# Kernel optimization log

Measured on AMD Instinct MI355X. Metric: run time of the kernel, lower is better.

Reference implementation:

```python
import jax, jax.numpy as jnp
import numpy as np
from jax import lax

K = 16
SIGMA2 = 1.0  # sigma=1.0 squared
EPS = 1e-06


def setup_inputs() -> dict:
    key = jax.random.key(0)
    xyz = jax.random.normal(key, (4, 3, 4096), dtype=jnp.float32)
    return {"xyz": xyz}


def reference(xyz):
    # xyz: (B, 3, N)
    B, _, N = xyz.shape
    pts = jnp.transpose(xyz, (0, 2, 1))  # (B, N, 3)

    sq = jnp.sum(pts * pts, axis=-1)  # (B, N)
    d2 = sq[:, :, None] + sq[:, None, :] - 2.0 * jnp.einsum("bnd,bmd->bnm", pts, pts)

    # k nearest neighbors (smallest distance, includes self like torch knn on same set)
    _, idx = lax.top_k(-d2, K)  # idx: (B, N, K)

    # gather neighbor coordinates and recompute exact squared distance (faithful to source)
    neighbors = jax.vmap(lambda p, i: p[i])(pts, idx)  # (B, N, K, 3)
    diff = pts[:, :, None, :] - neighbors
    dist2 = jnp.sum(diff * diff, axis=-1)  # (B, N, K)
    weights = jnp.exp(-dist2 / (2.0 * SIGMA2))

    # scatter k-sparse weights into dense adjacency (topk indices per row are unique)
    bb = jnp.arange(B)[:, None, None]
    ii = jnp.arange(N)[None, :, None]
    A = jnp.zeros((B, N, N), dtype=xyz.dtype).at[bb, ii, idx].set(weights)
    A = 0.5 * (A + jnp.swapaxes(A, 1, 2))

    # symmetric normalized Laplacian L = I - D^{-1/2} A D^{-1/2} (diag scaling via broadcast)
    D = jnp.clip(jnp.sum(A, axis=-1), EPS, None)
    d_is = D ** -0.5  # (B, N)
    L = jnp.eye(N, dtype=xyz.dtype)[None] - d_is[:, :, None] * A * d_is[:, None, :]
    return L
```

## Files before the change

kernel.cpp:

```cpp
#include <hip/hip_runtime.h>
#include <math.h>

#pragma clang fp contract(off)

#define NPTS 4096
#define KNN  16
#define RPBK 16
#define KT   1024
#define CAP  128

__device__ __forceinline__ unsigned okey(float f) {
    f = f + 0.0f;
    unsigned u = __float_as_uint(f);
    return u ^ (((unsigned)((int)u >> 31)) | 0x80000000u);
}

__device__ __forceinline__ unsigned wmin32(unsigned v) {
    for (int o = 32; o > 0; o >>= 1) { unsigned w = __shfl_xor(v, o); v = w < v ? w : v; }
    return v;
}
__device__ __forceinline__ unsigned long long wmin64(unsigned long long v) {
    for (int o = 32; o > 0; o >>= 1) { unsigned long long w = __shfl_xor(v, o); v = w < v ? w : v; }
    return v;
}

__global__ void zero_kernel(float* __restrict__ p, int n) {
    int i = blockIdx.x * blockDim.x + threadIdx.x;
    if (i < n) p[i] = 0.0f;
}

__global__ __launch_bounds__(KT, 8) void knn_kernel(const float* __restrict__ xyz,
                                                    float* __restrict__ Dsum,
                                                    int* __restrict__ idx_out,
                                                    float* __restrict__ w_out) {
    __shared__ float4 spts[NPTS];
    __shared__ int    lists[RPBK][CAP];

    const int t    = threadIdx.x;
    const int lane = t & 63;
    const int wv   = t >> 6;
    const int rowg = blockIdx.x * RPBK + wv;
    const int b    = rowg >> 12;
    const float* X = xyz + (size_t)b * 3 * NPTS;

    for (int i = t; i < NPTS; i += KT) {
        float x = X[i], y = X[NPTS + i], z = X[2 * NPTS + i];
        spts[i] = make_float4(x, y, z, (x * x + y * y) + z * z);
    }
    __syncthreads();

    const float4 P = spts[rowg & (NPTS - 1)];

    unsigned best1 = 0xFFFFFFFFu;
    for (int i = 0; i < NPTS / 64; ++i) {
        float4 Q  = spts[i * 64 + lane];
        float dot = (P.x * Q.x + P.y * Q.y) + P.z * Q.z;
        float d2  = (P.w + Q.w) - 2.0f * dot;
        unsigned k = okey(d2);
        best1 = k < best1 ? k : best1;
    }
    unsigned cur = best1, T = 0;
    for (int r = 0; r < KNN; ++r) {
        unsigned mn = wmin32(cur);
        T = mn;
        if (cur == mn) cur = 0xFFFFFFFFu;
    }

    int cnt = 0;
    for (int i = 0; i < NPTS / 64; ++i) {
        int m = i * 64 + lane;
        float4 Q  = spts[m];
        float dot = (P.x * Q.x + P.y * Q.y) + P.z * Q.z;
        float d2  = (P.w + Q.w) - 2.0f * dot;
        bool pass = okey(d2) <= T;
        unsigned long long bal = __ballot(pass);
        if (pass) {
            int pos = cnt + __popcll(bal & ((1ull << lane) - 1ull));
            if (pos < CAP) lists[wv][pos] = m;
        }
        cnt += (int)__popcll(bal);
    }

    unsigned long long sel = ~0ull;
    if (cnt <= CAP) {
        unsigned long long e0 = ~0ull, e1 = ~0ull;
        if (lane < cnt) {
            int m = lists[wv][lane]; float4 Q = spts[m];
            float dot = (P.x * Q.x + P.y * Q.y) + P.z * Q.z;
            float d2  = (P.w + Q.w) - 2.0f * dot;
            e0 = ((unsigned long long)okey(d2) << 32) | (unsigned)m;
        }
        if (lane + 64 < cnt) {
            int m = lists[wv][lane + 64]; float4 Q = spts[m];
            float dot = (P.x * Q.x + P.y * Q.y) + P.z * Q.z;
            float d2  = (P.w + Q.w) - 2.0f * dot;
            e1 = ((unsigned long long)okey(d2) << 32) | (unsigned)m;
        }
        unsigned long long c = e0 < e1 ? e0 : e1;
        for (int r = 0; r < KNN; ++r) {
            unsigned long long mn = wmin64(c);
            if (c == mn) {
                if (e0 == mn) e0 = ~0ull; else e1 = ~0ull;
                c = e0 < e1 ? e0 : e1;
            }
            if (lane == r) sel = mn;
        }
    } else {
        unsigned long long last = 0;
        for (int r = 0; r < KNN; ++r) {
            unsigned long long bestp = ~0ull;
            for (int i = 0; i < NPTS / 64; ++i) {
                int m = i * 64 + lane;
                float4 Q  = spts[m];
                float dot = (P.x * Q.x + P.y * Q.y) + P.z * Q.z;
                float d2  = (P.w + Q.w) - 2.0f * dot;
                unsigned long long key = ((unsigned long long)okey(d2) << 32) | (unsigned)m;
                if (key > last && key < bestp) bestp = key;
            }
            unsigned long long mn = wmin64(bestp);
            if (lane == r) sel = mn;
            last = mn;
        }
    }

    float wgt = 0.0f;
    if (lane < KNN) {
        int j = (int)(unsigned)(sel & 0xFFFFFFFFull);
        float4 Q = spts[j];
        float dx = P.x - Q.x, dy = P.y - Q.y, dz = P.z - Q.z;
        float dist2 = (dx * dx + dy * dy) + dz * dz;
        wgt = expf(-(dist2 * 0.5f));
        size_t base = (size_t)rowg * KNN + lane;
        idx_out[base] = j;
        w_out[base]   = wgt;
        atomicAdd(&Dsum[(b << 12) + j], 0.5f * wgt);
    }
    float rs = wgt;
    for (int o = 32; o > 0; o >>= 1) rs += __shfl_xor(rs, o);
    if (lane == 0) atomicAdd(&Dsum[rowg], 0.5f * rs);
}

__global__ void dis_kernel(const float* __restrict__ Dsum, float* __restrict__ dis, int n) {
    int i = blockIdx.x * blockDim.x + threadIdx.x;
    if (i < n) dis[i] = 1.0f / sqrtf(fmaxf(Dsum[i], 1e-6f));
}

__global__ __launch_bounds__(256) void fill_kernel(float4* __restrict__ L4, size_t T4) {
    size_t g4     = (size_t)blockIdx.x * blockDim.x + threadIdx.x;
    size_t stride = (size_t)gridDim.x * blockDim.x;
    for (; g4 < T4; g4 += stride) {
        size_t g = g4 << 2;
        int o    = (int)(g & (size_t)(NPTS * (size_t)NPTS - 1));
        int row  = o >> 12;
        int col0 = o & (NPTS - 1);
        float4 v;
        v.x = (row == col0    ) ? 1.0f : 0.0f;
        v.y = (row == col0 + 1) ? 1.0f : 0.0f;
        v.z = (row == col0 + 2) ? 1.0f : 0.0f;
        v.w = (row == col0 + 3) ? 1.0f : 0.0f;
        L4[g4] = v;
    }
}

__global__ __launch_bounds__(256) void scatter_kernel(const int* __restrict__ idxb,
                                                      const float* __restrict__ wb,
                                                      const float* __restrict__ dis,
                                                      float* __restrict__ L) {
    int g   = blockIdx.x * 256 + threadIdx.x;
    int row = g >> 4;
    int b   = row >> 12;
    int n   = row & (NPTS - 1);
    int j   = idxb[g];
    float v = -0.5f * wb[g] * dis[row] * dis[(b << 12) + j];
    float* Lb = L + (size_t)b * NPTS * NPTS;
    atomicAdd(Lb + (size_t)n * NPTS + j, v);
    atomicAdd(Lb + (size_t)j * NPTS + n, v);
}

extern "C" void kernel_launch(void* const* d_in, const int* in_sizes, int n_in,
                              void* d_out, int out_size, void* d_ws, size_t ws_size,
                              hipStream_t stream) {
    const float* xyz = (const float*)d_in[0];
    const int B  = in_sizes[0] / (3 * NPTS);
    const int BN = B * NPTS;

    float* Dsum = (float*)d_ws;
    float* dis  = Dsum + BN;
    int*   idxb = (int*)(dis + BN);
    float* wb   = (float*)(idxb + (size_t)BN * KNN);
    float* L    = (float*)d_out;

    zero_kernel<<<BN / 256, 256, 0, stream>>>(Dsum, BN);
    knn_kernel<<<BN / RPBK, KT, 0, stream>>>(xyz, Dsum, idxb, wb);
    dis_kernel<<<BN / 256, 256, 0, stream>>>(Dsum, dis, BN);
    size_t T4 = (size_t)B * NPTS * NPTS / 4;
    fill_kernel<<<8192, 256, 0, stream>>>((float4*)d_out, T4);
    scatter_kernel<<<(BN * KNN) / 256, 256, 0, stream>>>(idxb, wb, dis, L);
}
```

Baseline: 369.6 us.

## Process two rows per wave in kNN and fuse zero/dis kernels into neighbors

Each wave in the kNN kernel now handles two query rows, sharing each shared-memory point load across both distance computations in the threshold and filter passes. Blocks shrink to 8 waves. The Dsum zeroing moves into the fill kernel and the inverse-sqrt degree computation moves into the scatter kernel, removing two small launches. The risks are more register pressure per thread and a hardcoded zeroing size that assumes the batch fits in 4096 float4s.

```diff
diff --git a/kernel.cpp b/kernel.cpp
--- a/kernel.cpp
+++ b/kernel.cpp
@@ -5,8 +5,10 @@
 
 #define NPTS 4096
 #define KNN  16
-#define RPBK 16
-#define KT   1024
+#define RPW  2
+#define KWAVES 8
+#define KT   (KWAVES * 64)
+#define RPBK (KWAVES * RPW)
 #define CAP  128
 
 __device__ __forceinline__ unsigned okey(float f) {
@@ -24,130 +26,12 @@
     return v;
 }
 
-__global__ void zero_kernel(float* __restrict__ p, int n) {
-    int i = blockIdx.x * blockDim.x + threadIdx.x;
-    if (i < n) p[i] = 0.0f;
-}
-
-__global__ __launch_bounds__(KT, 8) void knn_kernel(const float* __restrict__ xyz,
-                                                    float* __restrict__ Dsum,
-                                                    int* __restrict__ idx_out,
-                                                    float* __restrict__ w_out) {
-    __shared__ float4 spts[NPTS];
-    __shared__ int    lists[RPBK][CAP];
-
-    const int t    = threadIdx.x;
-    const int lane = t & 63;
-    const int wv   = t >> 6;
-    const int rowg = blockIdx.x * RPBK + wv;
-    const int b    = rowg >> 12;
-    const float* X = xyz + (size_t)b * 3 * NPTS;
-
-    for (int i = t; i < NPTS; i += KT) {
-        float x = X[i], y = X[NPTS + i], z = X[2 * NPTS + i];
-        spts[i] = make_float4(x, y, z, (x * x + y * y) + z * z);
-    }
-    __syncthreads();
-
-    const float4 P = spts[rowg & (NPTS - 1)];
-
-    unsigned best1 = 0xFFFFFFFFu;
-    for (int i = 0; i < NPTS / 64; ++i) {
-        float4 Q  = spts[i * 64 + lane];
-        float dot = (P.x * Q.x + P.y * Q.y) + P.z * Q.z;
-        float d2  = (P.w + Q.w) - 2.0f * dot;
-        unsigned k = okey(d2);
-        best1 = k < best1 ? k : best1;
-    }
-    unsigned cur = best1, T = 0;
-    for (int r = 0; r < KNN; ++r) {
-        unsigned mn = wmin32(cur);
-        T = mn;
-        if (cur == mn) cur = 0xFFFFFFFFu;
-    }
-
-    int cnt = 0;
-    for (int i = 0; i < NPTS / 64; ++i) {
-        int m = i * 64 + lane;
-        float4 Q  = spts[m];
-        float dot = (P.x * Q.x + P.y * Q.y) + P.z * Q.z;
-        float d2  = (P.w + Q.w) - 2.0f * dot;
-        bool pass = okey(d2) <= T;
-        unsigned long long bal = __ballot(pass);
-        if (pass) {
-            int pos = cnt + __popcll(bal & ((1ull << lane) - 1ull));
-            if (pos < CAP) lists[wv][pos] = m;
-        }
-        cnt += (int)__popcll(bal);
-    }
-
-    unsigned long long sel = ~0ull;
-    if (cnt <= CAP) {
-        unsigned long long e0 = ~0ull, e1 = ~0ull;
-        if (lane < cnt) {
-            int m = lists[wv][lane]; float4 Q = spts[m];
-            float dot = (P.x * Q.x + P.y * Q.y) + P.z * Q.z;
-            float d2  = (P.w + Q.w) - 2.0f * dot;
-            e0 = ((unsigned long long)okey(d2) << 32) | (unsigned)m;
-        }
-        if (lane + 64 < cnt) {
-            int m = lists[wv][lane + 64]; float4 Q = spts[m];
-            float dot = (P.x * Q.x + P.y * Q.y) + P.z * Q.z;
-            float d2  = (P.w + Q.w) - 2.0f * dot;
-            e1 = ((unsigned long long)okey(d2) << 32) | (unsigned)m;
-        }
-        unsigned long long c = e0 < e1 ? e0 : e1;
-        for (int r = 0; r < KNN; ++r) {
-            unsigned long long mn = wmin64(c);
-            if (c == mn) {
-                if (e0 == mn) e0 = ~0ull; else e1 = ~0ull;
-                c = e0 < e1 ? e0 : e1;
-            }
-            if (lane == r) sel = mn;
-        }
-    } else {
-        unsigned long long last = 0;
-        for (int r = 0; r < KNN; ++r) {
-            unsigned long long bestp = ~0ull;
-            for (int i = 0; i < NPTS / 64; ++i) {
-                int m = i * 64 + lane;
-                float4 Q  = spts[m];
-                float dot = (P.x * Q.x + P.y * Q.y) + P.z * Q.z;
-                float d2  = (P.w + Q.w) - 2.0f * dot;
-                unsigned long long key = ((unsigned long long)okey(d2) << 32) | (unsigned)m;
-                if (key > last && key < bestp) bestp = key;
-            }
-            unsigned long long mn = wmin64(bestp);
-            if (lane == r) sel = mn;
-            last = mn;
-        }
-    }
-
-    float wgt = 0.0f;
-    if (lane < KNN) {
-        int j = (int)(unsigned)(sel & 0xFFFFFFFFull);
-        float4 Q = spts[j];
-        float dx = P.x - Q.x, dy = P.y - Q.y, dz = P.z - Q.z;
-        float dist2 = (dx * dx + dy * dy) + dz * dz;
-        wgt = expf(-(dist2 * 0.5f));
-        size_t base = (size_t)rowg * KNN + lane;
-        idx_out[base] = j;
-        w_out[base]   = wgt;
-        atomicAdd(&Dsum[(b << 12) + j], 0.5f * wgt);
-    }
-    float rs = wgt;
-    for (int o = 32; o > 0; o >>= 1) rs += __shfl_xor(rs, o);
-    if (lane == 0) atomicAdd(&Dsum[rowg], 0.5f * rs);
-}
-
-__global__ void dis_kernel(const float* __restrict__ Dsum, float* __restrict__ dis, int n) {
-    int i = blockIdx.x * blockDim.x + threadIdx.x;
-    if (i < n) dis[i] = 1.0f / sqrtf(fmaxf(Dsum[i], 1e-6f));
-}
-
-__global__ __launch_bounds__(256) void fill_kernel(float4* __restrict__ L4, size_t T4) {
+__global__ __launch_bounds__(256) void fill_kernel(float4* __restrict__ L4,
+                                                   float4* __restrict__ Dsum4,
+                                                   size_t T4) {
     size_t g4     = (size_t)blockIdx.x * blockDim.x + threadIdx.x;
     size_t stride = (size_t)gridDim.x * blockDim.x;
+    if (g4 < 4096) Dsum4[g4] = make_float4(0.f, 0.f, 0.f, 0.f);
     for (; g4 < T4; g4 += stride) {
         size_t g = g4 << 2;
         int o    = (int)(g & (size_t)(NPTS * (size_t)NPTS - 1));
@@ -162,16 +46,147 @@
     }
 }
 
+__global__ __launch_bounds__(KT, 4) void knn_kernel(const float* __restrict__ xyz,
+                                                    float* __restrict__ Dsum,
+                                                    int* __restrict__ idx_out,
+                                                    float* __restrict__ w_out) {
+    __shared__ float4 spts[NPTS];
+    __shared__ int    lists[RPBK][CAP];
+
+    const int t    = threadIdx.x;
+    const int lane = t & 63;
+    const int wv   = t >> 6;
+    const int row0 = blockIdx.x * RPBK + wv * RPW;
+    const int b    = row0 >> 12;
+    const float* X = xyz + (size_t)b * 3 * NPTS;
+
+    for (int i = t; i < NPTS; i += KT) {
+        float x = X[i], y = X[NPTS + i], z = X[2 * NPTS + i];
+        spts[i] = make_float4(x, y, z, (x * x + y * y) + z * z);
+    }
+    __syncthreads();
+
+    const float4 P0 = spts[(row0 + 0) & (NPTS - 1)];
+    const float4 P1 = spts[(row0 + 1) & (NPTS - 1)];
+
+    unsigned b0 = 0xFFFFFFFFu, b1 = 0xFFFFFFFFu;
+    for (int i = 0; i < NPTS / 64; ++i) {
+        float4 Q   = spts[i * 64 + lane];
+        float dot0 = (P0.x * Q.x + P0.y * Q.y) + P0.z * Q.z;
+        float dot1 = (P1.x * Q.x + P1.y * Q.y) + P1.z * Q.z;
+        unsigned k0 = okey((P0.w + Q.w) - 2.0f * dot0);
+        unsigned k1 = okey((P1.w + Q.w) - 2.0f * dot1);
+        b0 = k0 < b0 ? k0 : b0;
+        b1 = k1 < b1 ? k1 : b1;
+    }
+    unsigned T0 = 0, T1 = 0;
+    {
+        unsigned cur = b0;
+        for (int r = 0; r < KNN; ++r) { unsigned mn = wmin32(cur); T0 = mn; if (cur == mn) cur = 0xFFFFFFFFu; }
+        cur = b1;
+        for (int r = 0; r < KNN; ++r) { unsigned mn = wmin32(cur); T1 = mn; if (cur == mn) cur = 0xFFFFFFFFu; }
+    }
+
+    int cnt0 = 0, cnt1 = 0;
+    for (int i = 0; i < NPTS / 64; ++i) {
+        int m = i * 64 + lane;
+        float4 Q   = spts[m];
+        float dot0 = (P0.x * Q.x + P0.y * Q.y) + P0.z * Q.z;
+        float dot1 = (P1.x * Q.x + P1.y * Q.y) + P1.z * Q.z;
+        bool p0 = okey((P0.w + Q.w) - 2.0f * dot0) <= T0;
+        bool p1 = okey((P1.w + Q.w) - 2.0f * dot1) <= T1;
+        unsigned long long bal0 = __ballot(p0);
+        unsigned long long bal1 = __ballot(p1);
+        if (p0) {
+            int pos = cnt0 + __popcll(bal0 & ((1ull << lane) - 1ull));
+            if (pos < CAP) lists[wv * RPW + 0][pos] = m;
+        }
+        if (p1) {
+            int pos = cnt1 + __popcll(bal1 & ((1ull << lane) - 1ull));
+            if (pos < CAP) lists[wv * RPW + 1][pos] = m;
+        }
+        cnt0 += (int)__popcll(bal0);
+        cnt1 += (int)__popcll(bal1);
+    }
+
+    for (int r = 0; r < RPW; ++r) {
+        const int rowg = row0 + r;
+        const float4 P = r == 0 ? P0 : P1;
+        const int cnt  = r == 0 ? cnt0 : cnt1;
+        const int lr   = wv * RPW + r;
+
+        unsigned long long sel = ~0ull;
+        if (cnt <= CAP) {
+            unsigned long long e0 = ~0ull, e1 = ~0ull;
+            if (lane < cnt) {
+                int m = lists[lr][lane]; float4 Q = spts[m];
+                float dot = (P.x * Q.x + P.y * Q.y) + P.z * Q.z;
+                float d2  = (P.w + Q.w) - 2.0f * dot;
+                e0 = ((unsigned long long)okey(d2) << 32) | (unsigned)m;
+            }
+            if (lane + 64 < cnt) {
+                int m = lists[lr][lane + 64]; float4 Q = spts[m];
+                float dot = (P.x * Q.x + P.y * Q.y) + P.z * Q.z;
+                float d2  = (P.w + Q.w) - 2.0f * dot;
+                e1 = ((unsigned long long)okey(d2) << 32) | (unsigned)m;
+            }
+            unsigned long long c = e0 < e1 ? e0 : e1;
+            for (int k = 0; k < KNN; ++k) {
+                unsigned long long mn = wmin64(c);
+                if (c == mn) {
+                    if (e0 == mn) e0 = ~0ull; else e1 = ~0ull;
+                    c = e0 < e1 ? e0 : e1;
+                }
+                if (lane == k) sel = mn;
+            }
+        } else {
+            unsigned long long last = 0;
+            for (int k = 0; k < KNN; ++k) {
+                unsigned long long bestp = ~0ull;
+                for (int i = 0; i < NPTS / 64; ++i) {
+                    int m = i * 64 + lane;
+                    float4 Q  = spts[m];
+                    float dot = (P.x * Q.x + P.y * Q.y) + P.z * Q.z;
+                    float d2  = (P.w + Q.w) - 2.0f * dot;
+                    unsigned long long key = ((unsigned long long)okey(d2) << 32) | (unsigned)m;
+                    if (key > last && key < bestp) bestp = key;
+                }
+                unsigned long long mn = wmin64(bestp);
+                if (lane == k) sel = mn;
+                last = mn;
+            }
+        }
+
+        float wgt = 0.0f;
+        if (lane < KNN) {
+            int j = (int)(unsigned)(sel & 0xFFFFFFFFull);
+            float4 Q = spts[j];
+            float dx = P.x - Q.x, dy = P.y - Q.y, dz = P.z - Q.z;
+            float dist2 = (dx * dx + dy * dy) + dz * dz;
+            wgt = expf(-(dist2 * 0.5f));
+            size_t base = (size_t)rowg * KNN + lane;
+            idx_out[base] = j;
+            w_out[base]   = wgt;
+            atomicAdd(&Dsum[(b << 12) + j], 0.5f * wgt);
+        }
+        float rs = wgt;
+        for (int o = 32; o > 0; o >>= 1) rs += __shfl_xor(rs, o);
+        if (lane == 0) atomicAdd(&Dsum[rowg], 0.5f * rs);
+    }
+}
+
 __global__ __launch_bounds__(256) void scatter_kernel(const int* __restrict__ idxb,
                                                       const float* __restrict__ wb,
-                                                      const float* __restrict__ dis,
+                                                      const float* __restrict__ Dsum,
                                                       float* __restrict__ L) {
     int g   = blockIdx.x * 256 + threadIdx.x;
     int row = g >> 4;
     int b   = row >> 12;
     int n   = row & (NPTS - 1);
     int j   = idxb[g];
-    float v = -0.5f * wb[g] * dis[row] * dis[(b << 12) + j];
+    float sn = 1.0f / sqrtf(fmaxf(Dsum[row], 1e-6f));
+    float sj = 1.0f / sqrtf(fmaxf(Dsum[(b << 12) + j], 1e-6f));
+    float v  = -0.5f * wb[g] * sn * sj;
     float* Lb = L + (size_t)b * NPTS * NPTS;
     atomicAdd(Lb + (size_t)n * NPTS + j, v);
     atomicAdd(Lb + (size_t)j * NPTS + n, v);
@@ -185,15 +200,12 @@
     const int BN = B * NPTS;
 
     float* Dsum = (float*)d_ws;
-    float* dis  = Dsum + BN;
-    int*   idxb = (int*)(dis + BN);
+    int*   idxb = (int*)(Dsum + BN);
     float* wb   = (float*)(idxb + (size_t)BN * KNN);
     float* L    = (float*)d_out;
 
-    zero_kernel<<<BN / 256, 256, 0, stream>>>(Dsum, BN);
+    size_t T4 = (size_t)B * NPTS * NPTS / 4;
+    fill_kernel<<<8192, 256, 0, stream>>>((float4*)d_out, (float4*)Dsum, T4);
     knn_kernel<<<BN / RPBK, KT, 0, stream>>>(xyz, Dsum, idxb, wb);
-    dis_kernel<<<BN / 256, 256, 0, stream>>>(Dsum, dis, BN);
-    size_t T4 = (size_t)B * NPTS * NPTS / 4;
-    fill_kernel<<<8192, 256, 0, stream>>>((float4*)d_out, T4);
-    scatter_kernel<<<(BN * KNN) / 256, 256, 0, stream>>>(idxb, wb, dis, L);
-}
+    scatter_kernel<<<(BN * KNN) / 256, 256, 0, stream>>>(idxb, wb, Dsum, L);
+}
```

Result: no change. 371.2 us (+0.4%).
